# Kernel optimization log

Measured on AMD Instinct MI355X. Metric: run time of the kernel, lower is better.

## Reference

```python
import jax, jax.numpy as jnp
import numpy as np


def setup_inputs() -> dict:
    key = jax.random.key(0)
    doc_embeddings = jax.random.normal(key, (16384, 128), dtype=jnp.float32)
    return {"doc_embeddings": doc_embeddings}


def reference(doc_embeddings) -> jnp.ndarray:
    n = doc_embeddings.shape[0]
    # [N, N] pairwise dot products
    scores = jnp.matmul(doc_embeddings, doc_embeddings.T)
    positive_scores = jnp.diagonal(scores)  # [N]
    # zero out the diagonal (matches dot - eye*dot in the torch code)
    diag_mask = jnp.eye(n, dtype=scores.dtype)
    negative_scores = scores - diag_mask * scores
    positive_loss = jax.nn.log_sigmoid(positive_scores)            # [N]
    negative_loss = jax.nn.log_sigmoid(-negative_scores).sum(axis=1)  # [N]
    loss = -(positive_loss + negative_loss).mean()
    return loss
```

## Files before the change

### kernel.cpp

```cpp
#include <hip/hip_runtime.h>
#include <hip/hip_bf16.h>


#define N_DOCS 16384
#define DIM 128
#define NTILE 128
#define NTRI (NTILE * (NTILE + 1) / 2)
#define PBLOCKS 512

typedef __attribute__((ext_vector_type(4))) float f32x4;
typedef __attribute__((ext_vector_type(8))) __bf16 bf16x8;
typedef __attribute__((ext_vector_type(2))) long longx2;

typedef const __attribute__((address_space(1))) unsigned char* gptr_t;
typedef __attribute__((address_space(3))) unsigned char* lptr_t;

#define SQRT_LOG2E 1.2011224087864498f
#define LN2F 0.6931471805599453f
#define QC0 1.33985f
#define QC1 (-0.33985f)

#if __has_builtin(__builtin_amdgcn_exp2f)
#define EXP2F(x) __builtin_amdgcn_exp2f(x)
#else
#define EXP2F(x) exp2f(x)
#endif

#define BARRIER() do { asm volatile("" ::: "memory"); \
                       __builtin_amdgcn_s_barrier();  \
                       asm volatile("" ::: "memory"); } while (0)

__device__ __forceinline__ unsigned short f2bf(float f) {
  unsigned int u = __float_as_uint(f);
  u += 0x7fffu + ((u >> 16) & 1u);
  return (unsigned short)(u >> 16);
}

#if __has_builtin(__builtin_amdgcn_cvt_pk_fp8_f32)
#define HAVE_CVT_FP8 1
#else
__device__ __forceinline__ unsigned char f2e4m3(float x) {
  unsigned int u = __float_as_uint(x);
  unsigned char sgn = (unsigned char)((u >> 31) << 7);
  float ax = fabsf(x);
  if (!(ax < 464.f)) return sgn | 0x7E;
  unsigned int ua = u & 0x7FFFFFFFu;
  int e = (int)(ua >> 23) - 127;
  if (e < -6) {
    float q = rintf(ax * 512.f);
    return sgn | (unsigned char)q;
  }
  unsigned int mant = ua & 0x7FFFFFu;
  unsigned int keep = mant >> 20;
  unsigned int rest = mant & 0xFFFFFu;
  keep += (rest > 0x80000u) || (rest == 0x80000u && (keep & 1u));
  unsigned int ee = (unsigned int)(e + 7);
  if (keep == 8u) { keep = 0u; ee++; }
  if (ee >= 16u) return sgn | 0x7E;
  return sgn | (unsigned char)((ee << 3) | keep);
}
#endif

__device__ __forceinline__ void tri_decode(int g, int& tr, int& tc) {
  int r = (int)((2 * NTILE + 1 -
                 sqrtf((float)((2 * NTILE + 1) * (2 * NTILE + 1)) - 8.0f * (float)g)) * 0.5f);
  while (r * NTILE - r * (r - 1) / 2 > g) --r;
  while ((r + 1) * NTILE - (r + 1) * r / 2 <= g) ++r;
  tr = r;
  tc = r + (g - (r * NTILE - r * (r - 1) / 2));
}

__global__ void cast_kernel(const float* __restrict__ in, unsigned char* __restrict__ out,
                            float* __restrict__ accum) {
  int i = blockIdx.x * blockDim.x + threadIdx.x;
  if (i == 0) accum[0] = 0.f;
  int row = i >> 4, kb = i & 15;
  const float4* p = reinterpret_cast<const float4*>(in + (size_t)row * 128 + kb * 8);
  float4 a = p[0], b = p[1];
  int w0, w1;
#ifdef HAVE_CVT_FP8
  w0 = __builtin_amdgcn_cvt_pk_fp8_f32(a.x * SQRT_LOG2E, a.y * SQRT_LOG2E, 0, false);
  w0 = __builtin_amdgcn_cvt_pk_fp8_f32(a.z * SQRT_LOG2E, a.w * SQRT_LOG2E, w0, true);
  w1 = __builtin_amdgcn_cvt_pk_fp8_f32(b.x * SQRT_LOG2E, b.y * SQRT_LOG2E, 0, false);
  w1 = __builtin_amdgcn_cvt_pk_fp8_f32(b.z * SQRT_LOG2E, b.w * SQRT_LOG2E, w1, true);
#else
  w0 = (int)f2e4m3(a.x * SQRT_LOG2E) | ((int)f2e4m3(a.y * SQRT_LOG2E) << 8) |
       ((int)f2e4m3(a.z * SQRT_LOG2E) << 16) | ((int)f2e4m3(a.w * SQRT_LOG2E) << 24);
  w1 = (int)f2e4m3(b.x * SQRT_LOG2E) | ((int)f2e4m3(b.y * SQRT_LOG2E) << 8) |
       ((int)f2e4m3(b.z * SQRT_LOG2E) << 16) | ((int)f2e4m3(b.w * SQRT_LOG2E) << 24);
#endif
  int slab = row >> 7, r = row & 127, g = kb & 3, s = kb >> 2;
  int off = slab * 16384 + (g * 2 + (s >> 1)) * 2048 + r * 16 + (s & 1) * 8;
  *reinterpret_cast<int2*>(out + off) = make_int2(w0, w1);
}

__global__ __launch_bounds__(512, 4) void loss_persist(const unsigned char* __restrict__ ef8,
                                                       float* __restrict__ accum) {
  __shared__ alignas(16) unsigned char lds[2][2][16384];
  __shared__ float red[8];
  const int tid = threadIdx.x;
  const int p = blockIdx.x;
  const int nt = (NTRI - 1 - p) / PBLOCKS + 1;

  const int wid = tid >> 6;
  const int lane = tid & 63;
  const int wm = wid >> 2, wn = wid & 3;
  const int lrow = lane & 15;
  const int kgrp = lane >> 4;

  auto stage = [&](int g, int buf) {
    int tr, tc;
    tri_decode(g, tr, tc);
    const unsigned char* sA = ef8 + (size_t)tr * 16384;
    const unsigned char* sB = ef8 + (size_t)tc * 16384;
#pragma unroll
    for (int it = 0; it < 2; ++it) {
      int pp = (it * 512 + tid) * 16;
      __builtin_amdgcn_global_load_lds((gptr_t)(sA + pp),
                                       (lptr_t)((unsigned char*)lds[buf][0] + pp), 16, 0, 0);
      __builtin_amdgcn_global_load_lds((gptr_t)(sB + pp),
                                       (lptr_t)((unsigned char*)lds[buf][1] + pp), 16, 0, 0);
    }
  };

  auto compute = [&](int g, int buf) -> float {
    int tr, tc;
    tri_decode(g, tr, tc);
    const unsigned char* As = (const unsigned char*)lds[buf][0];
    const unsigned char* Bs = (const unsigned char*)lds[buf][1];

    f32x4 acc[4][2];
#pragma unroll
    for (int a = 0; a < 4; ++a)
#pragma unroll
      for (int c = 0; c < 2; ++c) acc[a][c] = (f32x4){0.f, 0.f, 0.f, 0.f};

#pragma unroll
    for (int ks2 = 0; ks2 < 2; ++ks2) {
      longx2 af[4], bf[2];
      const int pbase = (kgrp * 2 + ks2) * 2048;
#pragma unroll
      for (int f = 0; f < 4; ++f) {
        int ar = wm * 64 + f * 16 + lrow;
        af[f] = *reinterpret_cast<const longx2*>(As + pbase + ar * 16);
      }
#pragma unroll
      for (int f = 0; f < 2; ++f) {
        int br = wn * 32 + f * 16 + lrow;
        bf[f] = *reinterpret_cast<const longx2*>(Bs + pbase + br * 16);
      }
#pragma unroll
      for (int fm = 0; fm < 4; ++fm)
#pragma unroll
        for (int fn = 0; fn < 2; ++fn) {
          acc[fm][fn] = __builtin_amdgcn_mfma_f32_16x16x32_fp8_fp8(af[fm].x, bf[fn].x,
                                                                   acc[fm][fn], 0, 0, 0);
          acc[fm][fn] = __builtin_amdgcn_mfma_f32_16x16x32_fp8_fp8(af[fm].y, bf[fn].y,
                                                                   acc[fm][fn], 0, 0, 0);
        }
    }

    float sm = 0.f, sp = 0.f;
    if (tr == tc) {
#pragma unroll
      for (int fm = 0; fm < 4; ++fm)
#pragma unroll
        for (int fn = 0; fn < 2; ++fn)
#pragma unroll
          for (int r = 0; r < 4; ++r) {
            float v = acc[fm][fn][r];
            int il = wm * 64 + fm * 16 + kgrp * 4 + r;
            int jl = wn * 32 + fn * 16 + lrow;
            if (il == jl) v = -v;
            sm += fmaxf(v, 0.f);
            float u = EXP2F(-fabsf(v));
            sp = fmaf(u, fmaf(u, QC1, QC0), sp);
          }
      return sm + sp;
    } else {
#pragma unroll
      for (int fm = 0; fm < 4; ++fm)
#pragma unroll
        for (int fn = 0; fn < 2; ++fn)
#pragma unroll
          for (int r = 0; r < 4; ++r) {
            float v = acc[fm][fn][r];
            sm += fmaxf(v, 0.f);
            float u = EXP2F(-fabsf(v));
            sp = fmaf(u, fmaf(u, QC1, QC0), sp);
          }
      return 2.f * (sm + sp);
    }
  };

  float total = 0.f;
  int buf = 0;
  stage(p, 0);
  for (int i = 0; i < nt - 1; ++i) {
    stage(p + (i + 1) * PBLOCKS, buf ^ 1);
    asm volatile("s_waitcnt vmcnt(4)" ::: "memory");
    BARRIER();
    total += compute(p + i * PBLOCKS, buf);
    BARRIER();
    buf ^= 1;
  }
  asm volatile("s_waitcnt vmcnt(0)" ::: "memory");
  BARRIER();
  total += compute(p + (nt - 1) * PBLOCKS, buf);

#pragma unroll
  for (int off = 32; off > 0; off >>= 1) total += __shfl_down(total, off);
  if (lane == 0) red[wid] = total;
  __syncthreads();
  if (tid == 0) {
    float t = red[0] + red[1] + red[2] + red[3] + red[4] + red[5] + red[6] + red[7];
    atomicAdd(accum, t);
  }
}

__global__ __launch_bounds__(512, 2) void loss_fallback(const float* __restrict__ src,
                                                        float* __restrict__ accum) {
  const int b = blockIdx.x;
  int tr, tc;
  tri_decode(b, tr, tc);

  __shared__ alignas(16) unsigned short As[128 * 128];
  __shared__ alignas(16) unsigned short Bs[128 * 128];
  __shared__ float red[8];
  const int tid = threadIdx.x;

  const float4* srcA4 = (const float4*)(src + (size_t)tr * 16384);
  const float4* srcB4 = (const float4*)(src + (size_t)tc * 16384);
#pragma unroll
  for (int it = 0; it < 8; ++it) {
    int idx = it * 512 + tid;
    int L = idx * 8;
    int swz = L ^ (((L >> 8) & 7) << 4);
    float4 a = srcA4[idx];
    ushort4 oa = {f2bf(a.x * SQRT_LOG2E), f2bf(a.y * SQRT_LOG2E),
                  f2bf(a.z * SQRT_LOG2E), f2bf(a.w * SQRT_LOG2E)};
    *reinterpret_cast<ushort4*>((unsigned char*)As + swz) = oa;
    float4 bb = srcB4[idx];
    ushort4 ob = {f2bf(bb.x * SQRT_LOG2E), f2bf(bb.y * SQRT_LOG2E),
                  f2bf(bb.z * SQRT_LOG2E), f2bf(bb.w * SQRT_LOG2E)};
    *reinterpret_cast<ushort4*>((unsigned char*)Bs + swz) = ob;
  }
  __syncthreads();

  const int wid = tid >> 6;
  const int lane = tid & 63;
  const int wm = wid >> 2, wn = wid & 3;
  const int lrow = lane & 15;
  const int kgrp = lane >> 4;

  f32x4 acc[4][2];
#pragma unroll
  for (int a = 0; a < 4; ++a)
#pragma unroll
    for (int c = 0; c < 2; ++c) acc[a][c] = (f32x4){0.f, 0.f, 0.f, 0.f};

#pragma unroll
  for (int ks = 0; ks < 4; ++ks) {
    bf16x8 af[4], bfr[2];
#pragma unroll
    for (int f = 0; f < 4; ++f) {
      int ar = wm * 64 + f * 16 + lrow;
      int ab = (ar * 256 + ks * 64 + kgrp * 16) ^ ((ar & 7) << 4);
      af[f] = *reinterpret_cast<const bf16x8*>((const unsigned char*)As + ab);
    }
#pragma unroll
    for (int f = 0; f < 2; ++f) {
      int br = wn * 32 + f * 16 + lrow;
      int bb = (br * 256 + ks * 64 + kgrp * 16) ^ ((br & 7) << 4);
      bfr[f] = *reinterpret_cast<const bf16x8*>((const unsigned char*)Bs + bb);
    }
#pragma unroll
    for (int fm = 0; fm < 4; ++fm)
#pragma unroll
      for (int fn = 0; fn < 2; ++fn)
        acc[fm][fn] = __builtin_amdgcn_mfma_f32_16x16x32_bf16(af[fm], bfr[fn], acc[fm][fn], 0, 0, 0);
  }

  float sm = 0.f, sp = 0.f;
  if (tr == tc) {
#pragma unroll
    for (int fm = 0; fm < 4; ++fm)
#pragma unroll
      for (int fn = 0; fn < 2; ++fn)
#pragma unroll
        for (int r = 0; r < 4; ++r) {
          float v = acc[fm][fn][r];
          int il = wm * 64 + fm * 16 + kgrp * 4 + r;
          int jl = wn * 32 + fn * 16 + lrow;
          if (il == jl) v = -v;
          sm += fmaxf(v, 0.f);
          float u = EXP2F(-fabsf(v));
          sp = fmaf(u, fmaf(u, QC1, QC0), sp);
        }
  } else {
#pragma unroll
    for (int fm = 0; fm < 4; ++fm)
#pragma unroll
      for (int fn = 0; fn < 2; ++fn)
#pragma unroll
        for (int r = 0; r < 4; ++r) {
          float v = acc[fm][fn][r];
          sm += fmaxf(v, 0.f);
          float u = EXP2F(-fabsf(v));
          sp = fmaf(u, fmaf(u, QC1, QC0), sp);
        }
    sm *= 2.f;
    sp *= 2.f;
  }

  float lsum = sm + sp;
#pragma unroll
  for (int off = 32; off > 0; off >>= 1) lsum += __shfl_down(lsum, off);
  if (lane == 0) red[wid] = lsum;
  __syncthreads();
  if (tid == 0) {
    float t = red[0] + red[1] + red[2] + red[3] + red[4] + red[5] + red[6] + red[7];
    atomicAdd(accum, t);
  }
}

__global__ void finalize_kernel(const float* __restrict__ accum, float* __restrict__ out) {
  out[0] = LN2F * (accum[0] * (1.0f / (float)N_DOCS) + 1.0f);
}

extern "C" void kernel_launch(void* const* d_in, const int* in_sizes, int n_in,
                              void* d_out, int out_size, void* d_ws, size_t ws_size,
                              hipStream_t stream) {
  const float* E = (const float*)d_in[0];
  float* out = (float*)d_out;
  float* accum = (float*)d_ws;

  const size_t need = 256 + (size_t)N_DOCS * DIM;
  if (ws_size >= need) {
    unsigned char* ef8 = (unsigned char*)d_ws + 256;
    cast_kernel<<<(N_DOCS * (DIM / 8)) / 256, 256, 0, stream>>>(E, ef8, accum);
    loss_persist<<<PBLOCKS, 512, 0, stream>>>(ef8, accum);
  } else {
    (void)hipMemsetAsync(accum, 0, sizeof(float), stream);
    loss_fallback<<<NTRI, 512, 0, stream>>>(E, accum);
  }
  finalize_kernel<<<1, 1, 0, stream>>>(accum, out);
}
```

Baseline: 106.6 us.

## Use contiguous tile chunks with A-tile reuse, more blocks, and fused finalize

Each persistent block now processes a contiguous range of upper-triangular tile pairs. It keeps the row tile A resident in LDS and double-buffers only the B tile. This halves global-to-LDS traffic within a row and cuts per-block LDS, allowing more resident blocks (768 blocks, 6 per CU). The separate finalize kernel launch is replaced by a last-block-done atomic counter that writes the output. Row transitions load A and B without overlap, which adds exposed latency.

Result: no change. 107.8 us (+1.2%).

```diff
diff --git a/kernel.cpp b/kernel.cpp
--- a/kernel.cpp
+++ b/kernel.cpp
@@ -6,7 +6,7 @@
 #define DIM 128
 #define NTILE 128
 #define NTRI (NTILE * (NTILE + 1) / 2)
-#define PBLOCKS 512
+#define PBLOCKS 768
 
 typedef __attribute__((ext_vector_type(4))) float f32x4;
 typedef __attribute__((ext_vector_type(8))) __bf16 bf16x8;
@@ -71,9 +71,9 @@
 }
 
 __global__ void cast_kernel(const float* __restrict__ in, unsigned char* __restrict__ out,
-                            float* __restrict__ accum) {
+                            float* __restrict__ accum, unsigned int* __restrict__ counter) {
   int i = blockIdx.x * blockDim.x + threadIdx.x;
-  if (i == 0) accum[0] = 0.f;
+  if (i == 0) { accum[0] = 0.f; *counter = 0u; }
   int row = i >> 4, kb = i & 15;
   const float4* p = reinterpret_cast<const float4*>(in + (size_t)row * 128 + kb * 8);
   float4 a = p[0], b = p[1];
@@ -94,13 +94,18 @@
   *reinterpret_cast<int2*>(out + off) = make_int2(w0, w1);
 }
 
-__global__ __launch_bounds__(512, 4) void loss_persist(const unsigned char* __restrict__ ef8,
-                                                       float* __restrict__ accum) {
-  __shared__ alignas(16) unsigned char lds[2][2][16384];
+__global__ __launch_bounds__(512, 6) void loss_persist(const unsigned char* __restrict__ ef8,
+                                                       float* __restrict__ accum,
+                                                       unsigned int* __restrict__ counter,
+                                                       float* __restrict__ out) {
+  __shared__ alignas(16) unsigned char Asl[16384];
+  __shared__ alignas(16) unsigned char Bsl[2][16384];
   __shared__ float red[8];
   const int tid = threadIdx.x;
   const int p = blockIdx.x;
-  const int nt = (NTRI - 1 - p) / PBLOCKS + 1;
+  const int g0 = (p * 43) >> 2;
+  const int g1 = ((p + 1) * 43) >> 2;
+  const int n = g1 - g0;
 
   const int wid = tid >> 6;
   const int lane = tid & 63;
@@ -108,26 +113,26 @@
   const int lrow = lane & 15;
   const int kgrp = lane >> 4;
 
-  auto stage = [&](int g, int buf) {
-    int tr, tc;
-    tri_decode(g, tr, tc);
-    const unsigned char* sA = ef8 + (size_t)tr * 16384;
-    const unsigned char* sB = ef8 + (size_t)tc * 16384;
+  auto stageA = [&](int t) {
+    const unsigned char* s = ef8 + (size_t)t * 16384;
 #pragma unroll
     for (int it = 0; it < 2; ++it) {
       int pp = (it * 512 + tid) * 16;
-      __builtin_amdgcn_global_load_lds((gptr_t)(sA + pp),
-                                       (lptr_t)((unsigned char*)lds[buf][0] + pp), 16, 0, 0);
-      __builtin_amdgcn_global_load_lds((gptr_t)(sB + pp),
-                                       (lptr_t)((unsigned char*)lds[buf][1] + pp), 16, 0, 0);
+      __builtin_amdgcn_global_load_lds((gptr_t)(s + pp), (lptr_t)(Asl + pp), 16, 0, 0);
     }
   };
-
-  auto compute = [&](int g, int buf) -> float {
-    int tr, tc;
-    tri_decode(g, tr, tc);
-    const unsigned char* As = (const unsigned char*)lds[buf][0];
-    const unsigned char* Bs = (const unsigned char*)lds[buf][1];
+  auto stageB = [&](int t, int buf) {
+    const unsigned char* s = ef8 + (size_t)t * 16384;
+#pragma unroll
+    for (int it = 0; it < 2; ++it) {
+      int pp = (it * 512 + tid) * 16;
+      __builtin_amdgcn_global_load_lds((gptr_t)(s + pp), (lptr_t)(Bsl[buf] + pp), 16, 0, 0);
+    }
+  };
+
+  auto compute = [&](int buf, bool diag) -> float {
+    const unsigned char* As = (const unsigned char*)Asl;
+    const unsigned char* Bs = (const unsigned char*)Bsl[buf];
 
     f32x4 acc[4][2];
 #pragma unroll
@@ -161,7 +166,7 @@
     }
 
     float sm = 0.f, sp = 0.f;
-    if (tr == tc) {
+    if (diag) {
 #pragma unroll
       for (int fm = 0; fm < 4; ++fm)
 #pragma unroll
@@ -193,20 +198,32 @@
     }
   };
 
+  int tr, tc;
+  tri_decode(g0, tr, tc);
   float total = 0.f;
   int buf = 0;
-  stage(p, 0);
-  for (int i = 0; i < nt - 1; ++i) {
-    stage(p + (i + 1) * PBLOCKS, buf ^ 1);
-    asm volatile("s_waitcnt vmcnt(4)" ::: "memory");
+  stageA(tr);
+  stageB(tc, 0);
+  for (int i = 0; i < n; ++i) {
+    int ntr = tr, ntc = tc + 1;
+    if (ntc == NTILE) { ntr = tr + 1; ntc = ntr; }
+    const bool have_next = (i + 1 < n);
+    const bool samerow = have_next && (ntr == tr);
+    if (samerow) {
+      stageB(ntc, buf ^ 1);
+      asm volatile("s_waitcnt vmcnt(2)" ::: "memory");
+    } else {
+      asm volatile("s_waitcnt vmcnt(0)" ::: "memory");
+    }
     BARRIER();
-    total += compute(p + i * PBLOCKS, buf);
+    total += compute(buf, tr == tc);
     BARRIER();
-    buf ^= 1;
-  }
-  asm volatile("s_waitcnt vmcnt(0)" ::: "memory");
-  BARRIER();
-  total += compute(p + (nt - 1) * PBLOCKS, buf);
+    if (have_next && !samerow) {
+      stageA(ntr);
+      stageB(ntc, buf ^ 1);
+    }
+    tr = ntr; tc = ntc; buf ^= 1;
+  }
 
 #pragma unroll
   for (int off = 32; off > 0; off >>= 1) total += __shfl_down(total, off);
@@ -215,6 +232,12 @@
   if (tid == 0) {
     float t = red[0] + red[1] + red[2] + red[3] + red[4] + red[5] + red[6] + red[7];
     atomicAdd(accum, t);
+    __threadfence();
+    unsigned int old = atomicAdd(counter, 1u);
+    if (old == (unsigned int)(PBLOCKS - 1)) {
+      float v = atomicAdd(accum, 0.f);
+      out[0] = LN2F * (v * (1.0f / (float)N_DOCS) + 1.0f);
+    }
   }
 }
 
@@ -334,15 +357,16 @@
   const float* E = (const float*)d_in[0];
   float* out = (float*)d_out;
   float* accum = (float*)d_ws;
+  unsigned int* counter = (unsigned int*)((char*)d_ws + 64);
 
   const size_t need = 256 + (size_t)N_DOCS * DIM;
   if (ws_size >= need) {
     unsigned char* ef8 = (unsigned char*)d_ws + 256;
-    cast_kernel<<<(N_DOCS * (DIM / 8)) / 256, 256, 0, stream>>>(E, ef8, accum);
-    loss_persist<<<PBLOCKS, 512, 0, stream>>>(ef8, accum);
+    cast_kernel<<<(N_DOCS * (DIM / 8)) / 256, 256, 0, stream>>>(E, ef8, accum, counter);
+    loss_persist<<<PBLOCKS, 512, 0, stream>>>(ef8, accum, counter, out);
   } else {
     (void)hipMemsetAsync(accum, 0, sizeof(float), stream);
     loss_fallback<<<NTRI, 512, 0, stream>>>(E, accum);
-  }
-  finalize_kernel<<<1, 1, 0, stream>>>(accum, out);
-}
+    finalize_kernel<<<1, 1, 0, stream>>>(accum, out);
+  }
+}
```
